# Optimization experiments

Hardware: AMD Instinct MI355X
Metric: run time of the kernel (lower is better)

Reference implementation:

```python
import jax, jax.numpy as jnp
import numpy as np

N_COUPLES = 16      # 32 frames / tubelet-depth 2
GRID = 14           # 224 / 16 patches per row
CUBE = 9            # 729 = 9^3
VOL = (N_COUPLES * CUBE, GRID * CUBE, GRID * CUBE)  # (144, 126, 126)
OUT = (64, 64, 64)


def _nearest_idx(out_size, in_size):
    # torch F.interpolate(mode='nearest'): src = floor(dst * in/out)
    return jnp.floor(jnp.arange(out_size) * (in_size / out_size)).astype(jnp.int32)


def setup_inputs() -> dict:
    key = jax.random.key(0)
    hidden_states = jax.random.normal(key, (64, 3137, 768), dtype=jnp.float32)
    return {"hidden_states": hidden_states}


def reference(hidden_states) -> jnp.ndarray:
    B = hidden_states.shape[0]
    # drop CLS token -> [B, 3136, 768]
    x = hidden_states[:, 1:, :]
    # 1D nearest resize 768 -> 729 along feature dim
    x = x[:, :, _nearest_idx(CUBE ** 3, x.shape[-1])]  # [B, 3136, 729]
    # reverse_patching, fully vectorized:
    # token (couple i, row r, col p) with cube (d0,d1,d2) -> volume[9i+d0, 9r+d1, 9p+d2]
    v = x.reshape(B, N_COUPLES, GRID, GRID, CUBE, CUBE, CUBE)
    v = v.transpose(0, 1, 4, 2, 5, 3, 6).reshape(B, *VOL)  # [B, 144, 126, 126]
    # 3D nearest resize (144,126,126) -> (64,64,64)
    i0 = _nearest_idx(OUT[0], VOL[0])
    i1 = _nearest_idx(OUT[1], VOL[1])
    i2 = _nearest_idx(OUT[2], VOL[2])
    out = v[:, i0][:, :, i1][:, :, :, i2]  # [B, 64, 64, 64]
    return out[:, None]  # [B, 1, 64, 64, 64]
```

## Files before the change

kernel.cpp:

```cpp
#include <hip/hip_runtime.h>
#include <hip/hip_bf16.h>


#define TOKENS 3137
#define CHANNELS 768

__global__ __launch_bounds__(256) void gather4_swz_kernel(const float* __restrict__ in,
                                                          float* __restrict__ out) {
    const float ch_scale = (float)(768.0 / 729.0);

    int bid = blockIdx.x;
    int wg  = (bid & 7) * 2048 + (bid >> 3);

    int gid = wg * 256 + threadIdx.x;
    int o2 = gid & 63;
    int r  = gid >> 6;
    int o1 = r & 63;
    r >>= 6;
    int q  = r & 15;
    int b  = r >> 4;

    int i0 = (q  * 144) >> 6;
    int i1 = (o1 * 126) >> 6;
    int i2 = (o2 * 126) >> 6;

    int nq = i0 / 9, c0 = i0 - nq * 9;
    int g1 = i1 / 9, c1 = i1 - g1 * 9;
    int g2 = i2 / 9, c2 = i2 - g2 * 9;

    int cc = (c0 * 9 + c1) * 9 + c2;
    int ch = (int)floorf((float)cc * ch_scale);

    int t = 1 + (nq * 14 + g1) * 14 + g2;

    const float* src = in + ((long long)(b * TOKENS + t) * CHANNELS + ch);
    float v0 = src[0];
    float v1 = src[1 * 784 * CHANNELS];
    float v2 = src[2 * 784 * CHANNELS];
    float v3 = src[3 * 784 * CHANNELS];

    float* dst = out + ((((b << 6) | q) << 6 | o1) << 6 | o2);
    dst[0 << 16] = v0;
    dst[1 << 16] = v1;
    dst[2 << 16] = v2;
    dst[3 << 16] = v3;
}

extern "C" void kernel_launch(void* const* d_in, const int* in_sizes, int n_in,
                              void* d_out, int out_size, void* d_ws, size_t ws_size,
                              hipStream_t stream) {
    const float* in = (const float*)d_in[0];
    float* out = (float*)d_out;
    int blocks = 4194304 / 256;
    gather4_swz_kernel<<<blocks, 256, 0, stream>>>(in, out);
}
```

Baseline: 81.74 us.

## Assign each thread four depth outputs from the same token row

Each thread now handles the four output depth slices that fall inside one couple (same token, channel offsets 162*j) instead of four slices spaced 16 apart in depth. All four loads come from a single 768-float token row, and the four stores go to adjacent 4096-element planes. This targets gather locality: the four reads of a thread share a row in cache, where before they were spread across distant tokens. It relies on the depth mapping i0 = 9n + 2j holding exactly for the 144 to 64 resize.

```diff
diff --git a/kernel.cpp b/kernel.cpp
--- a/kernel.cpp
+++ b/kernel.cpp
@@ -5,7 +5,7 @@
 #define TOKENS 3137
 #define CHANNELS 768
 
-__global__ __launch_bounds__(256) void gather4_swz_kernel(const float* __restrict__ in,
+__global__ __launch_bounds__(256) void gather_row4_kernel(const float* __restrict__ in,
                                                           float* __restrict__ out) {
     const float ch_scale = (float)(768.0 / 729.0);
 
@@ -17,33 +17,32 @@
     int r  = gid >> 6;
     int o1 = r & 63;
     r >>= 6;
-    int q  = r & 15;
+    int n  = r & 15;
     int b  = r >> 4;
 
-    int i0 = (q  * 144) >> 6;
     int i1 = (o1 * 126) >> 6;
     int i2 = (o2 * 126) >> 6;
 
-    int nq = i0 / 9, c0 = i0 - nq * 9;
-    int g1 = i1 / 9, c1 = i1 - g1 * 9;
-    int g2 = i2 / 9, c2 = i2 - g2 * 9;
+    int g1 = i1 / 9, c1 = i1 - 9 * g1;
+    int g2 = i2 / 9, c2 = i2 - 9 * g2;
 
-    int cc = (c0 * 9 + c1) * 9 + c2;
-    int ch = (int)floorf((float)cc * ch_scale);
+    int cc0 = 9 * c1 + c2;
+    int t   = 1 + (n * 14 + g1) * 14 + g2;
 
-    int t = 1 + (nq * 14 + g1) * 14 + g2;
+    const float* row = in + (long long)(b * TOKENS + t) * CHANNELS;
 
-    const float* src = in + ((long long)(b * TOKENS + t) * CHANNELS + ch);
-    float v0 = src[0];
-    float v1 = src[1 * 784 * CHANNELS];
-    float v2 = src[2 * 784 * CHANNELS];
-    float v3 = src[3 * 784 * CHANNELS];
+    float v[4];
+    #pragma unroll
+    for (int j = 0; j < 4; ++j) {
+        int cc = 162 * j + cc0;
+        int ch = (int)floorf((float)cc * ch_scale);
+        v[j] = row[ch];
+    }
 
-    float* dst = out + ((((b << 6) | q) << 6 | o1) << 6 | o2);
-    dst[0 << 16] = v0;
-    dst[1 << 16] = v1;
-    dst[2 << 16] = v2;
-    dst[3 << 16] = v3;
+    float* dst = out + ((((long long)(b << 6) | (n << 2)) << 6 | o1) << 6 | o2);
+    #pragma unroll
+    for (int j = 0; j < 4; ++j)
+        dst[(long long)j << 12] = v[j];
 }
 
 extern "C" void kernel_launch(void* const* d_in, const int* in_sizes, int n_in,
@@ -52,5 +51,5 @@
     const float* in = (const float*)d_in[0];
     float* out = (float*)d_out;
     int blocks = 4194304 / 256;
-    gather4_swz_kernel<<<blocks, 256, 0, stream>>>(in, out);
+    gather_row4_kernel<<<blocks, 256, 0, stream>>>(in, out);
 }
```

Result: faster. 79.84 us (-2.3%).
